# Kernel tuning notes

Measured on AMD Instinct MI355X. Metric: run time of the kernel, lower is better.

Reference implementation:

```python
import jax, jax.numpy as jnp
import numpy as np

N_HEADS = 16
D_MODEL = 1024
HEAD_DIM = D_MODEL // N_HEADS
B, S = 2, 2048


def setup_inputs() -> dict:
    key = jax.random.key(0)
    ks = jax.random.split(key, 10)
    scale = 1.0 / np.sqrt(D_MODEL)
    inp = {
        "query_tokens": jax.random.normal(ks[0], (B, S, D_MODEL), dtype=jnp.float32),
        "key_or_value_tokens": jax.random.normal(ks[1], (B, S, D_MODEL), dtype=jnp.float32),
        "mask": jnp.ones((B, S, S), dtype=jnp.int32),
        "Wq": jax.random.normal(ks[2], (D_MODEL, D_MODEL), dtype=jnp.float32) * scale,
        "bq": jnp.zeros((D_MODEL,), dtype=jnp.float32),
        "Wk": jax.random.normal(ks[3], (D_MODEL, D_MODEL), dtype=jnp.float32) * scale,
        "bk": jnp.zeros((D_MODEL,), dtype=jnp.float32),
        "Wv": jax.random.normal(ks[4], (D_MODEL, D_MODEL), dtype=jnp.float32) * scale,
        "bv": jnp.zeros((D_MODEL,), dtype=jnp.float32),
        "Wo": jax.random.normal(ks[5], (D_MODEL, D_MODEL), dtype=jnp.float32) * scale,
        "bo": jnp.zeros((D_MODEL,), dtype=jnp.float32),
    }
    return inp


def reference(query_tokens, key_or_value_tokens, mask, Wq, bq, Wk, bk, Wv, bv, Wo, bo):
    b, s, d = query_tokens.shape
    h, dh = N_HEADS, HEAD_DIM

    def proj(x, W, bias):
        # torch Linear: x @ W.T + b ; then split heads -> (b, h, s, dh)
        y = jnp.einsum("bsd,ed->bse", x, W) + bias
        return y.reshape(b, -1, h, dh).transpose(0, 2, 1, 3)

    q = proj(query_tokens, Wq, bq)
    k = proj(key_or_value_tokens, Wk, bk)
    v = proj(key_or_value_tokens, Wv, bv)

    scores = jnp.einsum("bhqd,bhkd->bhqk", q, k) / jnp.sqrt(jnp.float32(dh))
    # mask: (b, Sq, Sk) -> (b, 1, Sq, Sk); zeros get large negative fill
    scores = jnp.where(mask[:, None, :, :] == 0, jnp.float32(-1e9), scores)
    attn = jax.nn.softmax(scores, axis=-1)
    out = jnp.einsum("bhqk,bhkd->bhqd", attn, v)
    out = out.transpose(0, 2, 1, 3).reshape(b, s, d)
    return jnp.einsum("bsd,ed->bse", out, Wo) + bo
```

## Files before the change

### kernel.cpp

```cpp
#include <hip/hip_runtime.h>
#include <hip/hip_bf16.h>

typedef __bf16 bf16_8  __attribute__((ext_vector_type(8)));
typedef __bf16 bf16_4  __attribute__((ext_vector_type(4)));
typedef float  f32_4   __attribute__((ext_vector_type(4)));

#define NH 16
#define DHD 64
#define BB 2
#define SS 2048
#define DD 1024

__device__ __forceinline__ void gload16(const __bf16* g, __bf16* l) {
    __builtin_amdgcn_global_load_lds(
        (const __attribute__((address_space(1))) void*)g,
        (__attribute__((address_space(3))) void*)l, 16, 0, 0);
}

__global__ __launch_bounds__(256) void conv_all(
    const float* __restrict__ s0, const float* __restrict__ s1,
    const float* __restrict__ s2, const float* __restrict__ s3,
    const float* __restrict__ s4, const float* __restrict__ s5,
    __bf16* __restrict__ d0, __bf16* __restrict__ d1, __bf16* __restrict__ d2,
    __bf16* __restrict__ d3, __bf16* __restrict__ d4, __bf16* __restrict__ d5) {
    const int y = blockIdx.y;
    if (y >= 2 && blockIdx.x >= 1024) return;
    const float* s = (y == 0) ? s0 : (y == 1) ? s1 : (y == 2) ? s2
                   : (y == 3) ? s3 : (y == 4) ? s4 : s5;
    __bf16* d      = (y == 0) ? d0 : (y == 1) ? d1 : (y == 2) ? d2
                   : (y == 3) ? d3 : (y == 4) ? d4 : d5;
    const int i = (blockIdx.x * 256 + threadIdx.x) * 4;
    f32_4 v = *(const f32_4*)&s[i];
    bf16_4 o; o[0] = (__bf16)v[0]; o[1] = (__bf16)v[1];
    o[2] = (__bf16)v[2]; o[3] = (__bf16)v[3];
    *(bf16_4*)&d[i] = o;
}

__global__ __launch_bounds__(256) void mask_flags_k(const int* __restrict__ mask,
                                                    int* __restrict__ flags) {
    const int id = blockIdx.x;
    const int b = id >> 10, qt = (id >> 5) & 31, kt = id & 31;
    const int t = threadIdx.x;
    const int row = t >> 2, seg = t & 3;
    const int* p = mask + ((size_t)b * SS + qt * 64 + row) * SS + kt * 64 + seg * 16;
    int any0 = 0;
#pragma unroll
    for (int i = 0; i < 4; ++i) {
        int4 v = *(const int4*)&p[i * 4];
        any0 |= (v.x == 0) | (v.y == 0) | (v.z == 0) | (v.w == 0);
    }
    unsigned long long bal = __ballot(any0);
    __shared__ int sf[4];
    if ((t & 63) == 0) sf[t >> 6] = (bal != 0ULL);
    __syncthreads();
    if (t == 0) flags[id] = sf[0] | sf[1] | sf[2] | sf[3];
}

template <int LAYOUT>
__device__ __forceinline__ void gemm_body(const __bf16* __restrict__ A,
                                          const __bf16* __restrict__ W,
                                          const float* __restrict__ bias,
                                          __bf16* __restrict__ out,
                                          __bf16* smem) {
    __bf16* ldsA0 = smem;
    __bf16* ldsB0 = smem + 4096;
    __bf16* ldsA1 = smem + 6144;
    __bf16* ldsB1 = smem + 10240;
    __bf16* ldsC  = smem;

    const int tid  = threadIdx.x;
    const int lane = tid & 63;
    const int w    = tid >> 6;
    const int quad = lane >> 4;
    const int l15  = lane & 15;
    const int wm   = w * 32;
    const int m0   = blockIdx.x * 128;
    const int n0   = blockIdx.y * 64;

    f32_4 acc[2][4] = {};

#define QSTAGE(KT, LA, LB)                                                     \
    do {                                                                       \
        _Pragma("unroll") for (int cc = 0; cc < 2; ++cc) {                     \
            const int c   = tid + cc * 256;                                    \
            const int row = c >> 2;                                            \
            const int cp  = c & 3;                                             \
            gload16(&A[(size_t)(m0 + row) * 1024 + (KT) + cp * 8],             \
                    &(LA)[c * 8]);                                             \
        }                                                                      \
        {                                                                      \
            const int c   = tid;                                               \
            const int row = c >> 2;                                            \
            const int cp  = c & 3;                                             \
            gload16(&W[(size_t)(n0 + row) * 1024 + (KT) + cp * 8],             \
                    &(LB)[c * 8]);                                             \
        }                                                                      \
    } while (0)

    QSTAGE(0, ldsA0, ldsB0);
    __syncthreads();

    for (int kt = 0; kt < 1024; kt += 32) {
        const int sel = (kt >> 5) & 1;
        const __bf16* la = sel ? ldsA1 : ldsA0;
        const __bf16* lb = sel ? ldsB1 : ldsB0;
        __bf16* na       = sel ? ldsA0 : ldsA1;
        __bf16* nb       = sel ? ldsB0 : ldsB1;
        if (kt + 32 < 1024) QSTAGE(kt + 32, na, nb);

        bf16_8 af[2], bfr[4];
#pragma unroll
        for (int i = 0; i < 2; ++i)
            af[i] = *(const bf16_8*)&la[(wm + i * 16 + l15) * 32 + quad * 8];
#pragma unroll
        for (int j = 0; j < 4; ++j)
            bfr[j] = *(const bf16_8*)&lb[(j * 16 + l15) * 32 + quad * 8];
#pragma unroll
        for (int i = 0; i < 2; ++i)
#pragma unroll
            for (int j = 0; j < 4; ++j)
                acc[i][j] = __builtin_amdgcn_mfma_f32_16x16x32_bf16(
                    af[i], bfr[j], acc[i][j], 0, 0, 0);

        __syncthreads();
    }
#undef QSTAGE

    if (LAYOUT == 2) {
#pragma unroll
        for (int i = 0; i < 2; ++i)
#pragma unroll
            for (int j = 0; j < 4; ++j) {
                const int col = n0 + j * 16 + l15;
                const float bv = bias[col];
                bf16_4 pk;
#pragma unroll
                for (int r = 0; r < 4; ++r) pk[r] = (__bf16)(acc[i][j][r] + bv);
                *(bf16_4*)&ldsC[(j * 16 + l15) * 136 + wm + i * 16 + quad * 4] = pk;
            }
        __syncthreads();
#pragma unroll
        for (int it = 0; it < 4; ++it) {
            const int g    = it * 256 + tid;
            const int colp = g >> 4;
            const int s8   = (g & 15) * 8;
            bf16_8 v = *(const bf16_8*)&ldsC[colp * 136 + s8];
            const int gcol = n0 + colp;
            const int grow = m0 + s8;
            *(bf16_8*)&out[(((size_t)(grow >> 11) * NH + (gcol >> 6)) * DHD +
                            (gcol & 63)) * SS + (grow & 2047)] = v;
        }
    } else {
#pragma unroll
        for (int i = 0; i < 2; ++i)
#pragma unroll
            for (int j = 0; j < 4; ++j) {
                const int col = n0 + j * 16 + l15;
                const float bv = bias[col];
#pragma unroll
                for (int r = 0; r < 4; ++r)
                    ldsC[(wm + i * 16 + quad * 4 + r) * 72 + j * 16 + l15] =
                        (__bf16)(acc[i][j][r] + bv);
            }
        __syncthreads();
#pragma unroll
        for (int it = 0; it < 4; ++it) {
            const int g   = it * 256 + tid;
            const int row = g >> 3;
            const int c8  = (g & 7) * 8;
            bf16_8 v = *(const bf16_8*)&ldsC[row * 72 + c8];
            const int grow = m0 + row;
            const int gcol = n0 + c8;
            *(bf16_8*)&out[(((size_t)(grow >> 11) * NH + (gcol >> 6)) * SS +
                            (grow & 2047)) * DHD + (gcol & 63)] = v;
        }
    }
}

__global__ __launch_bounds__(256) void gemm_qkv(
    const __bf16* __restrict__ Xq, const __bf16* __restrict__ Xkv,
    const __bf16* __restrict__ Wq, const float* __restrict__ bq,
    const __bf16* __restrict__ Wk, const float* __restrict__ bk,
    const __bf16* __restrict__ Wv, const float* __restrict__ bv,
    __bf16* __restrict__ Qo, __bf16* __restrict__ Ko, __bf16* __restrict__ VTo) {
    __shared__ __align__(16) __bf16 smem[12288];
    const int z = blockIdx.z;
    const __bf16* A    = (z == 0) ? Xq : Xkv;
    const __bf16* W    = (z == 0) ? Wq : (z == 1 ? Wk : Wv);
    const float* bias  = (z == 0) ? bq : (z == 1 ? bk : bv);
    if (z == 2)
        gemm_body<2>(A, W, bias, VTo, smem);
    else
        gemm_body<0>(A, W, bias, (z == 0) ? Qo : Ko, smem);
}

__global__ __launch_bounds__(256) void gemm_final(
    const __bf16* __restrict__ A, const __bf16* __restrict__ W,
    const float* __restrict__ bias, float* __restrict__ out) {
    __shared__ __align__(16) float smemf[128 * 68];
    __bf16* ldsA0 = (__bf16*)smemf;
    __bf16* ldsB0 = (__bf16*)smemf + 4096;
    __bf16* ldsA1 = (__bf16*)smemf + 6144;
    __bf16* ldsB1 = (__bf16*)smemf + 10240;
    float*  ldsC  = smemf;

    const int tid  = threadIdx.x;
    const int lane = tid & 63;
    const int w    = tid >> 6;
    const int quad = lane >> 4;
    const int l15  = lane & 15;
    const int wm   = w * 32;
    const int m0   = blockIdx.x * 128;
    const int n0   = blockIdx.y * 64;

    f32_4 acc[2][4] = {};

#define FSTAGE(KT, LA, LB)                                                     \
    do {                                                                       \
        _Pragma("unroll") for (int cc = 0; cc < 2; ++cc) {                     \
            const int c   = tid + cc * 256;                                    \
            const int row = c >> 2;                                            \
            const int cp  = c & 3;                                             \
            gload16(&A[(size_t)(m0 + row) * 1024 + (KT) + cp * 8],             \
                    &(LA)[c * 8]);                                             \
        }                                                                      \
        {                                                                      \
            const int c   = tid;                                               \
            const int row = c >> 2;                                            \
            const int cp  = c & 3;                                             \
            gload16(&W[(size_t)(n0 + row) * 1024 + (KT) + cp * 8],             \
                    &(LB)[c * 8]);                                             \
        }                                                                      \
    } while (0)

    FSTAGE(0, ldsA0, ldsB0);
    __syncthreads();

    for (int kt = 0; kt < 1024; kt += 32) {
        const int sel = (kt >> 5) & 1;
        const __bf16* la = sel ? ldsA1 : ldsA0;
        const __bf16* lb = sel ? ldsB1 : ldsB0;
        __bf16* na       = sel ? ldsA0 : ldsA1;
        __bf16* nb       = sel ? ldsB0 : ldsB1;
        if (kt + 32 < 1024) FSTAGE(kt + 32, na, nb);

        bf16_8 af[2], bfr[4];
#pragma unroll
        for (int i = 0; i < 2; ++i)
            af[i] = *(const bf16_8*)&la[(wm + i * 16 + l15) * 32 + quad * 8];
#pragma unroll
        for (int j = 0; j < 4; ++j)
            bfr[j] = *(const bf16_8*)&lb[(j * 16 + l15) * 32 + quad * 8];
#pragma unroll
        for (int i = 0; i < 2; ++i)
#pragma unroll
            for (int j = 0; j < 4; ++j)
                acc[i][j] = __builtin_amdgcn_mfma_f32_16x16x32_bf16(
                    af[i], bfr[j], acc[i][j], 0, 0, 0);

        __syncthreads();
    }
#undef FSTAGE

#pragma unroll
    for (int i = 0; i < 2; ++i)
#pragma unroll
        for (int j = 0; j < 4; ++j) {
            const int col = n0 + j * 16 + l15;
            const float bv = bias[col];
#pragma unroll
            for (int r = 0; r < 4; ++r)
                ldsC[(wm + i * 16 + quad * 4 + r) * 68 + j * 16 + l15] =
                    acc[i][j][r] + bv;
        }
    __syncthreads();
#pragma unroll
    for (int it = 0; it < 8; ++it) {
        const int g   = it * 256 + tid;
        const int row = g >> 4;
        const int c4  = (g & 15) * 4;
        f32_4 v = *(const f32_4*)&ldsC[row * 68 + c4];
        *(f32_4*)&out[(size_t)(m0 + row) * 1024 + n0 + c4] = v;
    }
}

__global__ __launch_bounds__(256, 2) void flash_attn(
    const __bf16* __restrict__ Q, const __bf16* __restrict__ K,
    const __bf16* __restrict__ VT, const int* __restrict__ mask,
    const int* __restrict__ flags, __bf16* __restrict__ O) {
    __shared__ __align__(16) __bf16 ldsK0[64 * 64];
    __shared__ __align__(16) __bf16 ldsK1[64 * 64];
    __shared__ __align__(16) __bf16 ldsV0[64 * 64];
    __shared__ __align__(16) __bf16 ldsV1[64 * 64];
    __shared__ __align__(16) __bf16 ldsP0[128 * 72];
    __shared__ __align__(16) __bf16 ldsP1[128 * 72];

    const int tid  = threadIdx.x;
    const int lane = tid & 63;
    const int w    = tid >> 6;
    const int quad = lane >> 4;
    const int l15  = lane & 15;
    const int q0   = blockIdx.x * 128;
    const int bh   = blockIdx.y;
    const int b    = bh >> 4;

    const __bf16* Qb  = Q + (size_t)bh * SS * DHD;
    const __bf16* Kb  = K + (size_t)bh * SS * DHD;
    const __bf16* VTb = VT + (size_t)bh * DHD * SS;
    const int*    mb  = mask + (size_t)b * SS * SS;
    const int*    flb = flags + (size_t)b * 1024 + blockIdx.x * 64;

    bf16_8 qa[2][2];
#pragma unroll
    for (int mt = 0; mt < 2; ++mt)
#pragma unroll
        for (int ks = 0; ks < 2; ++ks) {
            bf16_8 t = *(const bf16_8*)&Qb[(size_t)(q0 + w * 32 + mt * 16 + l15) * DHD +
                                           ks * 32 + quad * 8];
#pragma unroll
            for (int e = 0; e < 8; ++e)
                qa[mt][ks][e] = (__bf16)((float)t[e] * 0.18033688011112042f);
        }

    bf16_8 ones;
#pragma unroll
    for (int e = 0; e < 8; ++e) ones[e] = (__bf16)1.0f;

    f32_4 of[2][4] = {};
    f32_4 lsum[2] = {};

    const int c0 = tid, c1 = tid + 256;
    const int r_0 = c0 >> 3, r_1 = c1 >> 3;
    const int s_0 = (c0 & 7) ^ (r_0 & 7);
    const int s_1 = (c1 & 7) ^ (r_1 & 7);

#define STAGE_K(K0_, DST)                                                      \
    do {                                                                       \
        gload16(&Kb[(size_t)((K0_) + r_0) * DHD + s_0 * 8], &(DST)[c0 * 8]);   \
        gload16(&Kb[(size_t)((K0_) + r_1) * DHD + s_1 * 8], &(DST)[c1 * 8]);   \
    } while (0)
#define STAGE_V(K0_, DST)                                                      \
    do {                                                                       \
        gload16(&VTb[(size_t)r_0 * SS + (K0_) + s_0 * 8], &(DST)[c0 * 8]);     \
        gload16(&VTb[(size_t)r_1 * SS + (K0_) + s_1 * 8], &(DST)[c1 * 8]);     \
    } while (0)

    const int xq = l15 & 7;

#define QKT(KSRC, SA)                                                          \
    do {                                                                       \
        _Pragma("unroll") for (int ks = 0; ks < 2; ++ks) {                     \
            bf16_8 kb[4];                                                      \
            _Pragma("unroll") for (int j = 0; j < 4; ++j)                      \
                kb[j] = *(const bf16_8*)&(KSRC)[(j * 16 + l15) * 64 +          \
                                                (((ks * 4 + quad) ^ xq) * 8)]; \
            _Pragma("unroll") for (int mt = 0; mt < 2; ++mt)                   \
                _Pragma("unroll") for (int j = 0; j < 4; ++j)                  \
                    SA[mt][j] = __builtin_amdgcn_mfma_f32_16x16x32_bf16(       \
                        kb[j], qa[mt][ks], SA[mt][j], 0, 0, 0);                \
        }                                                                      \
    } while (0)

#define MASKF(TN, SA)                                                          \
    do {                                                                       \
        if ((flb[TN] | flb[32 + (TN)]) != 0) {                                 \
            _Pragma("unroll") for (int mt = 0; mt < 2; ++mt)                   \
                _Pragma("unroll") for (int j = 0; j < 4; ++j)                  \
                    _Pragma("unroll") for (int r = 0; r < 4; ++r) {            \
                        const int qg = q0 + w * 32 + mt * 16 + l15;            \
                        const int kg = (TN) * 64 + j * 16 + quad * 4 + r;      \
                        if (mb[(size_t)qg * SS + kg] == 0) SA[mt][j][r] = -1e9f; \
                    }                                                          \
        }                                                                      \
    } while (0)

#define EXPW(SA, PDST)                                                         \
    do {                                                                       \
        _Pragma("unroll") for (int mt = 0; mt < 2; ++mt)                       \
            _Pragma("unroll") for (int j = 0; j < 4; ++j) {                    \
                bf16_4 pk;                                                     \
                _Pragma("unroll") for (int r = 0; r < 4; ++r)                  \
                    pk[r] = (__bf16)__builtin_amdgcn_exp2f(SA[mt][j][r]);      \
                *(bf16_4*)&(PDST)[(w * 32 + mt * 16 + l15) * 72 + j * 16 +     \
                                  quad * 4] = pk;                              \
            }                                                                  \
    } while (0)

#define PV(VSRC, PSRC)                                                         \
    do {                                                                       \
        _Pragma("unroll") for (int ks2 = 0; ks2 < 2; ++ks2) {                  \
            bf16_8 pa[2], vb[4];                                               \
            _Pragma("unroll") for (int mt = 0; mt < 2; ++mt)                   \
                pa[mt] = *(const bf16_8*)&(PSRC)[(w * 32 + mt * 16 + l15) * 72 \
                                                 + ks2 * 32 + quad * 8];       \
            _Pragma("unroll") for (int jo = 0; jo < 4; ++jo)                   \
                vb[jo] = *(const bf16_8*)&(VSRC)[(jo * 16 + l15) * 64 +        \
                                                 (((ks2 * 4 + quad) ^ xq) * 8)]; \
            __builtin_amdgcn_s_setprio(1);                                     \
            _Pragma("unroll") for (int mt = 0; mt < 2; ++mt) {                 \
                _Pragma("unroll") for (int jo = 0; jo < 4; ++jo)               \
                    of[mt][jo] = __builtin_amdgcn_mfma_f32_16x16x32_bf16(      \
                        pa[mt], vb[jo], of[mt][jo], 0, 0, 0);                  \
                lsum[mt] = __builtin_amdgcn_mfma_f32_16x16x32_bf16(            \
                    pa[mt], ones, lsum[mt], 0, 0, 0);                          \
            }                                                                  \
            __builtin_amdgcn_s_setprio(0);                                     \
        }                                                                      \
    } while (0)

    STAGE_K(0, ldsK0);
    STAGE_V(0, ldsV0);
    __syncthreads();
    STAGE_K(64, ldsK1);
    STAGE_V(64, ldsV1);
    {
        f32_4 sa[2][4] = {};
        QKT(ldsK0, sa);
        MASKF(0, sa);
        EXPW(sa, ldsP0);
    }
    __syncthreads();

    for (int t = 0; t < 31; ++t) {
        const int sel = t & 1;
        __bf16* kst       = sel ? ldsK1 : ldsK0;
        const __bf16* kn  = sel ? ldsK0 : ldsK1;
        const __bf16* vc  = sel ? ldsV1 : ldsV0;
        const __bf16* pc  = sel ? ldsP1 : ldsP0;
        __bf16* pn        = sel ? ldsP0 : ldsP1;
        __bf16* vst       = sel ? ldsV1 : ldsV0;

        if (t < 30) STAGE_K((t + 2) * 64, kst);

        f32_4 sa[2][4] = {};
        QKT(kn, sa);
        MASKF(t + 1, sa);
        PV(vc, pc);
        EXPW(sa, pn);

        __syncthreads();
        if (t < 30) STAGE_V((t + 2) * 64, vst);
    }

    PV(ldsV1, ldsP1);

    const int hcol = (bh & 15) * 64;
#pragma unroll
    for (int mt = 0; mt < 2; ++mt)
#pragma unroll
        for (int r = 0; r < 4; ++r) {
            const float inv = 1.0f / fmaxf(lsum[mt][r], 1e-37f);
            const int qg = q0 + w * 32 + mt * 16 + quad * 4 + r;
#pragma unroll
            for (int jo = 0; jo < 4; ++jo)
                O[((size_t)b * SS + qg) * DD + hcol + jo * 16 + l15] =
                    (__bf16)(of[mt][jo][r] * inv);
        }
#undef STAGE_K
#undef STAGE_V
#undef QKT
#undef MASKF
#undef EXPW
#undef PV
}


extern "C" void kernel_launch(void* const* d_in, const int* in_sizes, int n_in,
                              void* d_out, int out_size, void* d_ws, size_t ws_size,
                              hipStream_t stream) {
    const float* xq   = (const float*)d_in[0];
    const float* xkv  = (const float*)d_in[1];
    const int*   mask = (const int*)d_in[2];
    const float* Wq   = (const float*)d_in[3];
    const float* bq   = (const float*)d_in[4];
    const float* Wk   = (const float*)d_in[5];
    const float* bk   = (const float*)d_in[6];
    const float* Wv   = (const float*)d_in[7];
    const float* bv   = (const float*)d_in[8];
    const float* Wo   = (const float*)d_in[9];
    const float* bo   = (const float*)d_in[10];

    __bf16* ws = (__bf16*)d_ws;
    const size_t big = (size_t)BB * SS * DD;
    const size_t wsz = (size_t)DD * DD;
    __bf16* Qw   = ws;
    __bf16* Kw   = Qw + big;
    __bf16* VTw  = Kw + big;
    __bf16* Aw   = VTw + big;
    __bf16* Xqb  = Aw + big;
    __bf16* Xkvb = Xqb + big;
    __bf16* Wqb  = Xkvb + big;
    __bf16* Wkb  = Wqb + wsz;
    __bf16* Wvb  = Wkb + wsz;
    __bf16* Wob  = Wvb + wsz;
    int* flags   = (int*)(Wob + wsz);

    conv_all<<<dim3(4096, 6), dim3(256), 0, stream>>>(xq, xkv, Wq, Wk, Wv, Wo,
                                                      Xqb, Xkvb, Wqb, Wkb, Wvb, Wob);
    mask_flags_k<<<dim3(2048), dim3(256), 0, stream>>>(mask, flags);
    gemm_qkv<<<dim3(32, 16, 3), dim3(256), 0, stream>>>(Xqb, Xkvb, Wqb, bq, Wkb, bk,
                                                        Wvb, bv, Qw, Kw, VTw);
    flash_attn<<<dim3(SS / 128, BB * NH), dim3(256), 0, stream>>>(Qw, Kw, VTw, mask,
                                                                  flags, Aw);
    gemm_final<<<dim3(32, 16), dim3(256), 0, stream>>>(Aw, Wob, bo, (float*)d_out);
}
```

Measured before the change: 230.9 us.

## Fuse mask-flag scan into conversion kernel and remap block IDs for XCD locality

Merges the mask tile-flag kernel into the fp32-to-bf16 conversion kernel as extra grid rows, removing one kernel launch. It also remaps linear block indices in the QKV GEMM, the output GEMM and flash attention so that blocks dispatched round-robin across the 8 XCDs get contiguous tiles. The aim is better L2 reuse of shared A/W tiles and K/V per head. The fused kernel launches empty blocks for the unused x range, and the remap assumes grid sizes divisible by 8.

Result: no change. 231.8 us (+0.4%).

```diff
diff --git a/kernel.cpp b/kernel.cpp
--- a/kernel.cpp
+++ b/kernel.cpp
@@ -17,13 +17,34 @@
         (__attribute__((address_space(3))) void*)l, 16, 0, 0);
 }
 
-__global__ __launch_bounds__(256) void conv_all(
+__global__ __launch_bounds__(256) void conv_mask(
     const float* __restrict__ s0, const float* __restrict__ s1,
     const float* __restrict__ s2, const float* __restrict__ s3,
     const float* __restrict__ s4, const float* __restrict__ s5,
     __bf16* __restrict__ d0, __bf16* __restrict__ d1, __bf16* __restrict__ d2,
-    __bf16* __restrict__ d3, __bf16* __restrict__ d4, __bf16* __restrict__ d5) {
+    __bf16* __restrict__ d3, __bf16* __restrict__ d4, __bf16* __restrict__ d5,
+    const int* __restrict__ mask, int* __restrict__ flags) {
     const int y = blockIdx.y;
+    if (y >= 6) {
+        if (blockIdx.x >= 1024) return;
+        const int id = (y - 6) * 1024 + blockIdx.x;
+        const int b = id >> 10, qt = (id >> 5) & 31, kt = id & 31;
+        const int t = threadIdx.x;
+        const int row = t >> 2, seg = t & 3;
+        const int* p = mask + ((size_t)b * SS + qt * 64 + row) * SS + kt * 64 + seg * 16;
+        int any0 = 0;
+#pragma unroll
+        for (int i = 0; i < 4; ++i) {
+            int4 v = *(const int4*)&p[i * 4];
+            any0 |= (v.x == 0) | (v.y == 0) | (v.z == 0) | (v.w == 0);
+        }
+        unsigned long long bal = __ballot(any0);
+        __shared__ int sf[4];
+        if ((t & 63) == 0) sf[t >> 6] = (bal != 0ULL);
+        __syncthreads();
+        if (t == 0) flags[id] = sf[0] | sf[1] | sf[2] | sf[3];
+        return;
+    }
     if (y >= 2 && blockIdx.x >= 1024) return;
     const float* s = (y == 0) ? s0 : (y == 1) ? s1 : (y == 2) ? s2
                    : (y == 3) ? s3 : (y == 4) ? s4 : s5;
@@ -36,32 +57,12 @@
     *(bf16_4*)&d[i] = o;
 }
 
-__global__ __launch_bounds__(256) void mask_flags_k(const int* __restrict__ mask,
-                                                    int* __restrict__ flags) {
-    const int id = blockIdx.x;
-    const int b = id >> 10, qt = (id >> 5) & 31, kt = id & 31;
-    const int t = threadIdx.x;
-    const int row = t >> 2, seg = t & 3;
-    const int* p = mask + ((size_t)b * SS + qt * 64 + row) * SS + kt * 64 + seg * 16;
-    int any0 = 0;
-#pragma unroll
-    for (int i = 0; i < 4; ++i) {
-        int4 v = *(const int4*)&p[i * 4];
-        any0 |= (v.x == 0) | (v.y == 0) | (v.z == 0) | (v.w == 0);
-    }
-    unsigned long long bal = __ballot(any0);
-    __shared__ int sf[4];
-    if ((t & 63) == 0) sf[t >> 6] = (bal != 0ULL);
-    __syncthreads();
-    if (t == 0) flags[id] = sf[0] | sf[1] | sf[2] | sf[3];
-}
-
 template <int LAYOUT>
 __device__ __forceinline__ void gemm_body(const __bf16* __restrict__ A,
                                           const __bf16* __restrict__ W,
                                           const float* __restrict__ bias,
                                           __bf16* __restrict__ out,
-                                          __bf16* smem) {
+                                          __bf16* smem, int m0, int n0) {
     __bf16* ldsA0 = smem;
     __bf16* ldsB0 = smem + 4096;
     __bf16* ldsA1 = smem + 6144;
@@ -74,8 +75,6 @@
     const int quad = lane >> 4;
     const int l15  = lane & 15;
     const int wm   = w * 32;
-    const int m0   = blockIdx.x * 128;
-    const int n0   = blockIdx.y * 64;
 
     f32_4 acc[2][4] = {};
 
@@ -184,14 +183,18 @@
     const __bf16* __restrict__ Wv, const float* __restrict__ bv,
     __bf16* __restrict__ Qo, __bf16* __restrict__ Ko, __bf16* __restrict__ VTo) {
     __shared__ __align__(16) __bf16 smem[12288];
-    const int z = blockIdx.z;
+    const int p  = blockIdx.x + 32 * (blockIdx.y + 16 * blockIdx.z);
+    const int l  = (p & 7) * 192 + (p >> 3);
+    const int xm = l & 31;
+    const int yn = (l >> 5) & 15;
+    const int z  = l >> 9;
     const __bf16* A    = (z == 0) ? Xq : Xkv;
     const __bf16* W    = (z == 0) ? Wq : (z == 1 ? Wk : Wv);
     const float* bias  = (z == 0) ? bq : (z == 1 ? bk : bv);
     if (z == 2)
-        gemm_body<2>(A, W, bias, VTo, smem);
+        gemm_body<2>(A, W, bias, VTo, smem, xm * 128, yn * 64);
     else
-        gemm_body<0>(A, W, bias, (z == 0) ? Qo : Ko, smem);
+        gemm_body<0>(A, W, bias, (z == 0) ? Qo : Ko, smem, xm * 128, yn * 64);
 }
 
 __global__ __launch_bounds__(256) void gemm_final(
@@ -210,8 +213,10 @@
     const int quad = lane >> 4;
     const int l15  = lane & 15;
     const int wm   = w * 32;
-    const int m0   = blockIdx.x * 128;
-    const int n0   = blockIdx.y * 64;
+    const int p   = blockIdx.x + 32 * blockIdx.y;
+    const int lg  = (p & 7) * 64 + (p >> 3);
+    const int m0  = (lg & 31) * 128;
+    const int n0  = (lg >> 5) * 64;
 
     f32_4 acc[2][4] = {};
 
@@ -300,15 +305,18 @@
     const int w    = tid >> 6;
     const int quad = lane >> 4;
     const int l15  = lane & 15;
-    const int q0   = blockIdx.x * 128;
-    const int bh   = blockIdx.y;
-    const int b    = bh >> 4;
+    const int p   = blockIdx.x + 16 * blockIdx.y;
+    const int lg  = (p & 7) * 64 + (p >> 3);
+    const int qx  = lg & 15;
+    const int bh  = lg >> 4;
+    const int q0  = qx * 128;
+    const int b   = bh >> 4;
 
     const __bf16* Qb  = Q + (size_t)bh * SS * DHD;
     const __bf16* Kb  = K + (size_t)bh * SS * DHD;
     const __bf16* VTb = VT + (size_t)bh * DHD * SS;
     const int*    mb  = mask + (size_t)b * SS * SS;
-    const int*    flb = flags + (size_t)b * 1024 + blockIdx.x * 64;
+    const int*    flb = flags + (size_t)b * 1024 + qx * 64;
 
     bf16_8 qa[2][2];
 #pragma unroll
@@ -495,9 +503,9 @@
     __bf16* Wob  = Wvb + wsz;
     int* flags   = (int*)(Wob + wsz);
 
-    conv_all<<<dim3(4096, 6), dim3(256), 0, stream>>>(xq, xkv, Wq, Wk, Wv, Wo,
-                                                      Xqb, Xkvb, Wqb, Wkb, Wvb, Wob);
-    mask_flags_k<<<dim3(2048), dim3(256), 0, stream>>>(mask, flags);
+    conv_mask<<<dim3(4096, 8), dim3(256), 0, stream>>>(xq, xkv, Wq, Wk, Wv, Wo,
+                                                       Xqb, Xkvb, Wqb, Wkb, Wvb, Wob,
+                                                       mask, flags);
     gemm_qkv<<<dim3(32, 16, 3), dim3(256), 0, stream>>>(Xqb, Xkvb, Wqb, bq, Wkb, bk,
                                                         Wvb, bv, Qw, Kw, VTw);
     flash_attn<<<dim3(SS / 128, BB * NH), dim3(256), 0, stream>>>(Qw, Kw, VTw, mask,
```

## Fuse mask-flag pass into conversion kernel and deepen QKV GEMM K-tile with swizzle

Applied to the files above, without the earlier changes.

Merges the mask-flag scan into the fp32->bf16 conversion launch as extra grid rows, removing one kernel launch. The QKV GEMM now stages 64-wide K slices instead of 32, halving the number of loop iterations and barriers. It also XOR-swizzles the LDS layout to avoid bank conflicts on fragment reads. LDS use doubles to 48KB per block, which may reduce occupancy.

New measurement: 220.1 us. 4.7% less time.

```diff
diff --git a/kernel.cpp b/kernel.cpp
--- a/kernel.cpp
+++ b/kernel.cpp
@@ -17,13 +17,34 @@
         (__attribute__((address_space(3))) void*)l, 16, 0, 0);
 }
 
-__global__ __launch_bounds__(256) void conv_all(
+__global__ __launch_bounds__(256) void conv_mask(
     const float* __restrict__ s0, const float* __restrict__ s1,
     const float* __restrict__ s2, const float* __restrict__ s3,
     const float* __restrict__ s4, const float* __restrict__ s5,
     __bf16* __restrict__ d0, __bf16* __restrict__ d1, __bf16* __restrict__ d2,
-    __bf16* __restrict__ d3, __bf16* __restrict__ d4, __bf16* __restrict__ d5) {
+    __bf16* __restrict__ d3, __bf16* __restrict__ d4, __bf16* __restrict__ d5,
+    const int* __restrict__ mask, int* __restrict__ flags) {
     const int y = blockIdx.y;
+    if (y >= 6) {
+        if (blockIdx.x >= 1024) return;
+        const int id = (y - 6) * 1024 + blockIdx.x;
+        const int b = id >> 10, qt = (id >> 5) & 31, kt = id & 31;
+        const int t = threadIdx.x;
+        const int row = t >> 2, seg = t & 3;
+        const int* p = mask + ((size_t)b * SS + qt * 64 + row) * SS + kt * 64 + seg * 16;
+        int any0 = 0;
+#pragma unroll
+        for (int i = 0; i < 4; ++i) {
+            int4 v = *(const int4*)&p[i * 4];
+            any0 |= (v.x == 0) | (v.y == 0) | (v.z == 0) | (v.w == 0);
+        }
+        unsigned long long bal = __ballot(any0);
+        __shared__ int sf[4];
+        if ((t & 63) == 0) sf[t >> 6] = (bal != 0ULL);
+        __syncthreads();
+        if (t == 0) flags[id] = sf[0] | sf[1] | sf[2] | sf[3];
+        return;
+    }
     if (y >= 2 && blockIdx.x >= 1024) return;
     const float* s = (y == 0) ? s0 : (y == 1) ? s1 : (y == 2) ? s2
                    : (y == 3) ? s3 : (y == 4) ? s4 : s5;
@@ -36,36 +57,16 @@
     *(bf16_4*)&d[i] = o;
 }
 
-__global__ __launch_bounds__(256) void mask_flags_k(const int* __restrict__ mask,
-                                                    int* __restrict__ flags) {
-    const int id = blockIdx.x;
-    const int b = id >> 10, qt = (id >> 5) & 31, kt = id & 31;
-    const int t = threadIdx.x;
-    const int row = t >> 2, seg = t & 3;
-    const int* p = mask + ((size_t)b * SS + qt * 64 + row) * SS + kt * 64 + seg * 16;
-    int any0 = 0;
-#pragma unroll
-    for (int i = 0; i < 4; ++i) {
-        int4 v = *(const int4*)&p[i * 4];
-        any0 |= (v.x == 0) | (v.y == 0) | (v.z == 0) | (v.w == 0);
-    }
-    unsigned long long bal = __ballot(any0);
-    __shared__ int sf[4];
-    if ((t & 63) == 0) sf[t >> 6] = (bal != 0ULL);
-    __syncthreads();
-    if (t == 0) flags[id] = sf[0] | sf[1] | sf[2] | sf[3];
-}
-
 template <int LAYOUT>
 __device__ __forceinline__ void gemm_body(const __bf16* __restrict__ A,
                                           const __bf16* __restrict__ W,
                                           const float* __restrict__ bias,
                                           __bf16* __restrict__ out,
-                                          __bf16* smem) {
+                                          __bf16* smem, int m0, int n0) {
     __bf16* ldsA0 = smem;
-    __bf16* ldsB0 = smem + 4096;
-    __bf16* ldsA1 = smem + 6144;
-    __bf16* ldsB1 = smem + 10240;
+    __bf16* ldsB0 = smem + 8192;
+    __bf16* ldsA1 = smem + 12288;
+    __bf16* ldsB1 = smem + 20480;
     __bf16* ldsC  = smem;
 
     const int tid  = threadIdx.x;
@@ -74,25 +75,24 @@
     const int quad = lane >> 4;
     const int l15  = lane & 15;
     const int wm   = w * 32;
-    const int m0   = blockIdx.x * 128;
-    const int n0   = blockIdx.y * 64;
+    const int xq   = l15 & 7;
 
     f32_4 acc[2][4] = {};
 
 #define QSTAGE(KT, LA, LB)                                                     \
     do {                                                                       \
+        _Pragma("unroll") for (int cc = 0; cc < 4; ++cc) {                     \
+            const int c   = tid + cc * 256;                                    \
+            const int row = c >> 3;                                            \
+            const int sg  = (c & 7) ^ (row & 7);                               \
+            gload16(&A[(size_t)(m0 + row) * 1024 + (KT) + sg * 8],             \
+                    &(LA)[c * 8]);                                             \
+        }                                                                      \
         _Pragma("unroll") for (int cc = 0; cc < 2; ++cc) {                     \
             const int c   = tid + cc * 256;                                    \
-            const int row = c >> 2;                                            \
-            const int cp  = c & 3;                                             \
-            gload16(&A[(size_t)(m0 + row) * 1024 + (KT) + cp * 8],             \
-                    &(LA)[c * 8]);                                             \
-        }                                                                      \
-        {                                                                      \
-            const int c   = tid;                                               \
-            const int row = c >> 2;                                            \
-            const int cp  = c & 3;                                             \
-            gload16(&W[(size_t)(n0 + row) * 1024 + (KT) + cp * 8],             \
+            const int row = c >> 3;                                            \
+            const int sg  = (c & 7) ^ (row & 7);                               \
+            gload16(&W[(size_t)(n0 + row) * 1024 + (KT) + sg * 8],             \
                     &(LB)[c * 8]);                                             \
         }                                                                      \
     } while (0)
@@ -100,27 +100,32 @@
     QSTAGE(0, ldsA0, ldsB0);
     __syncthreads();
 
-    for (int kt = 0; kt < 1024; kt += 32) {
-        const int sel = (kt >> 5) & 1;
+    for (int kt = 0; kt < 1024; kt += 64) {
+        const int sel = (kt >> 6) & 1;
         const __bf16* la = sel ? ldsA1 : ldsA0;
         const __bf16* lb = sel ? ldsB1 : ldsB0;
         __bf16* na       = sel ? ldsA0 : ldsA1;
         __bf16* nb       = sel ? ldsB0 : ldsB1;
-        if (kt + 32 < 1024) QSTAGE(kt + 32, na, nb);
-
-        bf16_8 af[2], bfr[4];
-#pragma unroll
-        for (int i = 0; i < 2; ++i)
-            af[i] = *(const bf16_8*)&la[(wm + i * 16 + l15) * 32 + quad * 8];
-#pragma unroll
-        for (int j = 0; j < 4; ++j)
-            bfr[j] = *(const bf16_8*)&lb[(j * 16 + l15) * 32 + quad * 8];
-#pragma unroll
-        for (int i = 0; i < 2; ++i)
+        if (kt + 64 < 1024) QSTAGE(kt + 64, na, nb);
+
+#pragma unroll
+        for (int ks = 0; ks < 2; ++ks) {
+            bf16_8 af[2], bfr[4];
+#pragma unroll
+            for (int i = 0; i < 2; ++i)
+                af[i] = *(const bf16_8*)&la[(wm + i * 16 + l15) * 64 +
+                                            (((ks * 4 + quad) ^ xq) * 8)];
 #pragma unroll
             for (int j = 0; j < 4; ++j)
-                acc[i][j] = __builtin_amdgcn_mfma_f32_16x16x32_bf16(
-                    af[i], bfr[j], acc[i][j], 0, 0, 0);
+                bfr[j] = *(const bf16_8*)&lb[(j * 16 + l15) * 64 +
+                                             (((ks * 4 + quad) ^ xq) * 8)];
+#pragma unroll
+            for (int i = 0; i < 2; ++i)
+#pragma unroll
+                for (int j = 0; j < 4; ++j)
+                    acc[i][j] = __builtin_amdgcn_mfma_f32_16x16x32_bf16(
+                        af[i], bfr[j], acc[i][j], 0, 0, 0);
+        }
 
         __syncthreads();
     }
@@ -183,15 +188,16 @@
     const __bf16* __restrict__ Wk, const float* __restrict__ bk,
     const __bf16* __restrict__ Wv, const float* __restrict__ bv,
     __bf16* __restrict__ Qo, __bf16* __restrict__ Ko, __bf16* __restrict__ VTo) {
-    __shared__ __align__(16) __bf16 smem[12288];
+    __shared__ __align__(16) __bf16 smem[24576];
     const int z = blockIdx.z;
     const __bf16* A    = (z == 0) ? Xq : Xkv;
     const __bf16* W    = (z == 0) ? Wq : (z == 1 ? Wk : Wv);
     const float* bias  = (z == 0) ? bq : (z == 1 ? bk : bv);
     if (z == 2)
-        gemm_body<2>(A, W, bias, VTo, smem);
+        gemm_body<2>(A, W, bias, VTo, smem, blockIdx.x * 128, blockIdx.y * 64);
     else
-        gemm_body<0>(A, W, bias, (z == 0) ? Qo : Ko, smem);
+        gemm_body<0>(A, W, bias, (z == 0) ? Qo : Ko, smem,
+                     blockIdx.x * 128, blockIdx.y * 64);
 }
 
 __global__ __launch_bounds__(256) void gemm_final(
@@ -495,9 +501,9 @@
     __bf16* Wob  = Wvb + wsz;
     int* flags   = (int*)(Wob + wsz);
 
-    conv_all<<<dim3(4096, 6), dim3(256), 0, stream>>>(xq, xkv, Wq, Wk, Wv, Wo,
-                                                      Xqb, Xkvb, Wqb, Wkb, Wvb, Wob);
-    mask_flags_k<<<dim3(2048), dim3(256), 0, stream>>>(mask, flags);
+    conv_mask<<<dim3(4096, 8), dim3(256), 0, stream>>>(xq, xkv, Wq, Wk, Wv, Wo,
+                                                       Xqb, Xkvb, Wqb, Wkb, Wvb, Wob,
+                                                       mask, flags);
     gemm_qkv<<<dim3(32, 16, 3), dim3(256), 0, stream>>>(Xqb, Xkvb, Wqb, bq, Wkb, bk,
                                                         Wvb, bv, Qw, Kw, VTw);
     flash_attn<<<dim3(SS / 128, BB * NH), dim3(256), 0, stream>>>(Qw, Kw, VTw, mask,
```
